# Kernel tuning notes

Hardware: AMD Instinct MI355X
Metric: run time of the kernel (lower is better)

The kernel has to match this reference:

```python
import jax, jax.numpy as jnp
import numpy as np

B, S, D = 1, 2048, 2048
HQ, HKV = 32, 8
HD = D // HQ          # 64
G = HQ // HKV         # 4 query heads per kv head


def apply_rope(x, freq):
    # x: (b, h, s, hd); freq: (s, hd//2) angles. Llama-style pairwise rotation.
    cos = jnp.cos(freq)  # (s, hd//2)
    sin = jnp.sin(freq)
    xr = x.reshape(*x.shape[:-1], HD // 2, 2)
    xe, xo = xr[..., 0], xr[..., 1]
    re = xe * cos - xo * sin
    ro = xe * sin + xo * cos
    return jnp.stack([re, ro], axis=-1).reshape(x.shape)


def setup_inputs() -> dict:
    key = jax.random.key(0)
    k1, k2, k3, k4, k5 = jax.random.split(key, 5)
    x = jax.random.normal(k1, (B, S, D), dtype=jnp.float32)
    # RoPE angles: pos * inv_freq, theta=10000
    inv_freq = 1.0 / (10000.0 ** (jnp.arange(0, HD, 2, dtype=jnp.float32) / HD))
    freq = jnp.arange(S, dtype=jnp.float32)[:, None] * inv_freq[None, :]  # (S, HD//2)
    mask = jnp.tril(jnp.ones((S, S), dtype=jnp.int32))
    scale = D ** -0.5
    wq = jax.random.normal(k2, (D, HQ * HD), dtype=jnp.float32) * scale
    wk = jax.random.normal(k3, (D, HKV * HD), dtype=jnp.float32) * scale
    wv = jax.random.normal(k4, (D, HKV * HD), dtype=jnp.float32) * scale
    wo = jax.random.normal(k5, (HQ * HD, D), dtype=jnp.float32) * scale
    return {"x": x, "freq": freq, "mask": mask, "wq": wq, "wk": wk, "wv": wv, "wo": wo}


def reference(x, freq, mask, wq, wk, wv, wo):
    b, s, d = x.shape
    q = (x @ wq).reshape(b, s, HQ, HD).transpose(0, 2, 1, 3)    # (b,HQ,s,hd)
    k = (x @ wk).reshape(b, s, HKV, HD).transpose(0, 2, 1, 3)   # (b,HKV,s,hd)
    v = (x @ wv).reshape(b, s, HKV, HD).transpose(0, 2, 1, 3)
    q = apply_rope(q, freq[:s])
    k = apply_rope(k, freq[:s])
    # GQA: broadcast kv heads over groups instead of repeat_interleave
    qg = q.reshape(b, HKV, G, s, HD)
    scores = jnp.einsum('bhgsd,bhtd->bhgst', qg, k)             # (b,HKV,G,s,s)
    scores = jnp.where(mask[:s, :s] == 0, -jnp.inf, scores)
    w = jax.nn.softmax(scores * (HD ** -0.5), axis=-1)
    out = jnp.einsum('bhgst,bhtd->bhgsd', w, v)
    out = out.reshape(b, HQ, s, HD).transpose(0, 2, 1, 3).reshape(b, s, HQ * HD)
    return out @ wo
```

## Files before the change

### kernel.cpp

```cpp
#include <hip/hip_runtime.h>

typedef unsigned short u16;
typedef unsigned int u32;
typedef unsigned long long u64;

using bf16x8 = __bf16 __attribute__((ext_vector_type(8)));
using f32x4  = float  __attribute__((ext_vector_type(4)));

#define LDS_SPACE __attribute__((address_space(3)))
#define GLB_SPACE __attribute__((address_space(1)))

static __device__ __forceinline__ u16 f2bf(float f) {
  union { float f; u32 u; } c; c.f = f;
  u32 u = c.u;
  return (u16)((u + 0x7fffu + ((u >> 16) & 1u)) >> 16);
}
static __device__ __forceinline__ float bf2f(u16 u) {
  union { u32 u; float f; } c; c.u = ((u32)u) << 16;
  return c.f;
}

static __device__ __forceinline__ void fence_barrier() {
  asm volatile("" ::: "memory");
  __builtin_amdgcn_s_barrier();
  asm volatile("" ::: "memory");
}

constexpr float SC = 0.18033688011112042f;

__device__ __constant__ unsigned char kItems[40] = {
  12, 28, 29, 42, 44, 45, 46, 57, 59, 60, 61, 62, 63,
  24, 25, 37, 38, 40, 41, 49, 51, 52, 53, 54, 55, 56, 58,
  8, 20, 21, 32, 33, 34, 36, 48, 50,
  16, 17,
  4,
  0
};

__global__ __launch_bounds__(256) void prep_k(const float* __restrict__ x,
                                              const float* __restrict__ wq,
                                              const float* __restrict__ wk,
                                              const float* __restrict__ wv,
                                              const float* __restrict__ wo,
                                              u16* __restrict__ x_bf,
                                              u16* __restrict__ wqkv_t,
                                              u16* __restrict__ wo_t) {
  const int b = blockIdx.x;
  if (b < 4096) {
    int i = b * 256 + threadIdx.x;
    float4 v = ((const float4*)x)[i];
    ushort4 o;
    o.x = f2bf(v.x); o.y = f2bf(v.y); o.z = f2bf(v.z); o.w = f2bf(v.w);
    ((ushort4*)x_bf)[i] = o;
    return;
  }
  const float* src; u16* dst; int C, bx, by; float scale = 1.0f;
  if (b < 8192)      { src = wq; dst = wqkv_t; C = 2048; int t = b - 4096; bx = t & 63; by = t >> 6; scale = SC; }
  else if (b < 9216) { src = wk; dst = wqkv_t + (size_t)2048 * 2048; C = 512; int t = b - 8192; bx = t & 15; by = t >> 4; }
  else if (b < 10240){ src = wv; dst = wqkv_t + (size_t)2560 * 2048; C = 512; int t = b - 9216; bx = t & 15; by = t >> 4; }
  else               { src = wo; dst = wo_t; C = 2048; int t = b - 10240; bx = t & 63; by = t >> 6; }
  __shared__ float t[32][33];
  const int lx = threadIdx.x & 31, ly = threadIdx.x >> 5;
  const int r0 = by * 32, c0 = bx * 32;
  #pragma unroll
  for (int i = 0; i < 32; i += 8)
    t[ly + i][lx] = src[(size_t)(r0 + ly + i) * C + c0 + lx];
  __syncthreads();
  #pragma unroll
  for (int i = 0; i < 32; i += 8)
    dst[(size_t)(c0 + ly + i) * 2048 + r0 + lx] = f2bf(t[lx][ly + i] * scale);
}

__global__ __launch_bounds__(256) void ropevt_k(u16* __restrict__ Y,
                                                const float* __restrict__ freq,
                                                u16* __restrict__ Vt) {
  const int b = blockIdx.x;
  if (b < 10240) {
    int idx = b * 256 + threadIdx.x;
    int s = idx / 1280;
    int rem = idx - s * 1280;
    int h = rem >> 5;
    int i = rem & 31;
    int col = (h < 32) ? (h * 64 + 2 * i) : (2048 + (h - 32) * 64 + 2 * i);
    float ang = freq[s * 32 + i];
    float sn, cs;
    sincosf(ang, &sn, &cs);
    size_t base = (size_t)s * 3072 + col;
    float e = bf2f(Y[base]), o = bf2f(Y[base + 1]);
    Y[base]     = f2bf(e * cs - o * sn);
    Y[base + 1] = f2bf(e * sn + o * cs);
    return;
  }
  __shared__ u16 t[64][72];
  const int tb = b - 10240;
  const int s0 = (tb & 31) * 64;
  const int c0 = (tb >> 5) * 64;
  const int lx = threadIdx.x & 63, ly = threadIdx.x >> 6;
  #pragma unroll
  for (int i = 0; i < 64; i += 4)
    t[i + ly][lx] = Y[(size_t)(s0 + i + ly) * 3072 + 2560 + c0 + lx];
  __syncthreads();
  #pragma unroll
  for (int i = 0; i < 64; i += 4)
    Vt[(size_t)(c0 + i + ly) * 2048 + s0 + lx] = t[lx][i + ly];
}

template <typename OutT, int BN, int GX>
__global__ __launch_bounds__(256) void gemm64_k(const u16* __restrict__ A,
                                                const u16* __restrict__ Bt,
                                                OutT* __restrict__ C,
                                                int M, int N, int K) {
  constexpr int WN = BN / 32;
  __shared__ u16 As[2][64 * 64];
  __shared__ u16 Bs[2][BN * 64];
  const int tid = threadIdx.x, lane = tid & 63, w = tid >> 6;
  const int wr = w >> 1, wc = w & 1;
  const int nwg = gridDim.x;
  const int bsw = (blockIdx.x & 7) * (nwg >> 3) + ((int)blockIdx.x >> 3);
  const int bm = bsw / GX, bn = bsw - bm * GX;
  const int l15 = lane & 15, lq = lane >> 4;
  f32x4 acc[2][WN] = {};

  const int srow8 = lane >> 3;
  const int scolb = ((lane & 7) ^ srow8) * 16;
  const u16* AgR = A + (size_t)(bm * 64 + w * 16 + srow8) * K;
  const u16* BgR = Bt + (size_t)(bn * BN + w * (BN / 4) + srow8) * K;

  auto stage = [&](int buf, int k0) {
    #pragma unroll
    for (int i = 0; i < 2; ++i)
      __builtin_amdgcn_global_load_lds(
          (const GLB_SPACE u32*)((const char*)(AgR + (size_t)i * 8 * K + k0) + scolb),
          (LDS_SPACE u32*)&As[buf][(w * 16 + i * 8) * 64], 16, 0, 0);
    #pragma unroll
    for (int i = 0; i < WN; ++i)
      __builtin_amdgcn_global_load_lds(
          (const GLB_SPACE u32*)((const char*)(BgR + (size_t)i * 8 * K + k0) + scolb),
          (LDS_SPACE u32*)&Bs[buf][(w * (BN / 4) + i * 8) * 64], 16, 0, 0);
  };

  stage(0, 0);
  asm volatile("s_waitcnt vmcnt(0)" ::: "memory");
  fence_barrier();

  for (int k0 = 0; k0 < K; k0 += 64) {
    const int p = (k0 >> 6) & 1;
    if (k0 + 64 < K) stage(p ^ 1, k0 + 64);

    #pragma unroll
    for (int kk = 0; kk < 2; ++kk) {
      bf16x8 a[2], b[WN];
      #pragma unroll
      for (int m = 0; m < 2; ++m) {
        const int ra = wr * 32 + m * 16 + l15;
        a[m] = *(const bf16x8*)&As[p][ra * 64 + (((kk * 4 + lq) ^ (ra & 7)) << 3)];
      }
      #pragma unroll
      for (int n = 0; n < WN; ++n) {
        const int rb = wc * (BN / 2) + n * 16 + l15;
        b[n] = *(const bf16x8*)&Bs[p][rb * 64 + (((kk * 4 + lq) ^ (rb & 7)) << 3)];
      }
      #pragma unroll
      for (int m = 0; m < 2; ++m)
        #pragma unroll
        for (int n = 0; n < WN; ++n)
          acc[m][n] = __builtin_amdgcn_mfma_f32_16x16x32_bf16(a[m], b[n], acc[m][n], 0, 0, 0);
    }

    asm volatile("s_waitcnt vmcnt(0)" ::: "memory");
    fence_barrier();
  }

  const int r0 = bm * 64 + wr * 32 + lq * 4;
  const int c0 = bn * BN + wc * (BN / 2) + l15;
  #pragma unroll
  for (int m = 0; m < 2; ++m)
    #pragma unroll
    for (int n = 0; n < WN; ++n)
      #pragma unroll
      for (int r = 0; r < 4; ++r) {
        float v = acc[m][n][r];
        size_t off = (size_t)(r0 + m * 16 + r) * N + (c0 + n * 16);
        if constexpr (sizeof(OutT) == 2) ((u16*)C)[off] = f2bf(v);
        else C[off] = v;
      }
}

__global__ __launch_bounds__(256, 3) void attn_part_k(const u16* __restrict__ Y,
                                                      const u16* __restrict__ Vtg,
                                                      u16* __restrict__ Opart,
                                                      float2* __restrict__ Ml,
                                                      u16* __restrict__ Out) {
  __shared__ u16 Ks[64 * 64];
  __shared__ u16 Vs[64 * 64];
  __shared__ u32 Ps[4][16 * 32];
  const int w = threadIdx.x >> 6, lane = threadIdx.x & 63;
  const int l15 = lane & 15, lq = lane >> 4;

  const int b = (int)blockIdx.x;
  const int head = b & 31;
  const int idx = b >> 5;
  const int v = kItems[idx];
  const int qt = v >> 2, ch = v & 3;
  const int kvh = head >> 2;
  const int ntiles = 2 * qt + 2;
  const int nch = qt < 4 ? 1 : qt < 8 ? 2 : qt < 12 ? 3 : 4;
  const int tstart = (ch * ntiles) / nch;
  const int tend = ((ch + 1) * ntiles) / nch;
  const int q0w = qt * 128 + w * 32;

  const int srow = lane >> 3;
  const int scolb = ((lane & 7) ^ srow) * 16;
  const char* gkB = (const char*)(Y + (size_t)(w * 16 + srow) * 3072 + 2048 + kvh * 64) + scolb;
  const char* gvB = (const char*)(Vtg + (size_t)(kvh * 64 + w * 16 + srow) * 2048) + scolb;

  auto stage = [&](int t) {
    const size_t t0 = (size_t)t * 64;
    #pragma unroll
    for (int i = 0; i < 2; ++i) {
      __builtin_amdgcn_global_load_lds((const GLB_SPACE u32*)(gkB + t0 * 6144 + (size_t)i * 49152),
                                       (LDS_SPACE u32*)&Ks[(w * 16 + i * 8) * 64], 16, 0, 0);
      __builtin_amdgcn_global_load_lds((const GLB_SPACE u32*)(gvB + t0 * 2 + (size_t)i * 32768),
                                       (LDS_SPACE u32*)&Vs[(w * 16 + i * 8) * 64], 16, 0, 0);
    }
  };

  int rowB[4], xk[2], pwr[4], prd[2];
  #pragma unroll
  for (int kt = 0; kt < 4; ++kt) rowB[kt] = (kt * 16 + l15) * 128;
  #pragma unroll
  for (int kk = 0; kk < 2; ++kk) xk[kk] = (((kk * 4 + lq) ^ (l15 & 7)) << 4);
  #pragma unroll
  for (int n = 0; n < 4; ++n)
    pwr[n] = (l15 * 32 + ((lq * 2 + n * 8) ^ ((l15 & 7) << 2))) * 4;
  #pragma unroll
  for (int c = 0; c < 2; ++c)
    prd[c] = l15 * 128 + (((c * 32 + lq * 8) ^ ((l15 & 7) << 3)) << 1);

  bf16x8 qf[2][2];
  #pragma unroll
  for (int qs = 0; qs < 2; ++qs)
    #pragma unroll
    for (int kk = 0; kk < 2; ++kk)
      qf[qs][kk] = *(const bf16x8*)&Y[(size_t)(q0w + qs * 16 + l15) * 3072 +
                                      head * 64 + kk * 32 + lq * 8];

  float m_[2] = { -1e30f, -1e30f };
  float l_[2] = { 0.f, 0.f };
  f32x4 accO[2][4] = {};

  for (int t = tstart; t < tend; ++t) {
    stage(t);
    asm volatile("s_waitcnt vmcnt(0)" ::: "memory");
    fence_barrier();

    const int t0 = t * 64;
    if (t0 <= q0w + 31) {
      const char* KbC = (const char*)Ks;
      const char* VbC = (const char*)Vs;

      f32x4 sc[2][4] = {};
      #pragma unroll
      for (int kk = 0; kk < 2; ++kk)
        #pragma unroll
        for (int kt = 0; kt < 4; ++kt) {
          bf16x8 a = *(const bf16x8*)(KbC + rowB[kt] + xk[kk]);
          sc[0][kt] = __builtin_amdgcn_mfma_f32_16x16x32_bf16(a, qf[0][kk], sc[0][kt], 0, 0, 0);
          sc[1][kt] = __builtin_amdgcn_mfma_f32_16x16x32_bf16(a, qf[1][kk], sc[1][kt], 0, 0, 0);
        }

      bf16x8 vf[2][4];
      #pragma unroll
      for (int c = 0; c < 2; ++c)
        #pragma unroll
        for (int dt = 0; dt < 4; ++dt)
          vf[c][dt] = *(const bf16x8*)(VbC + rowB[dt] + xk[c]);

      #pragma unroll
      for (int qs = 0; qs < 2; ++qs) {
        const int qsmin = q0w + qs * 16;
        if (t0 > qsmin + 15) continue;
        const int qrow = qsmin + l15;
        if (t0 + 63 > qsmin) {
          #pragma unroll
          for (int n = 0; n < 4; ++n)
            #pragma unroll
            for (int rr = 0; rr < 4; ++rr)
              if (t0 + n * 16 + lq * 4 + rr > qrow) sc[qs][n][rr] = -1e30f;
        }
        float a0 = fmaxf(fmaxf(sc[qs][0][0], sc[qs][0][1]), fmaxf(sc[qs][0][2], sc[qs][0][3]));
        float a1 = fmaxf(fmaxf(sc[qs][1][0], sc[qs][1][1]), fmaxf(sc[qs][1][2], sc[qs][1][3]));
        float a2 = fmaxf(fmaxf(sc[qs][2][0], sc[qs][2][1]), fmaxf(sc[qs][2][2], sc[qs][2][3]));
        float a3 = fmaxf(fmaxf(sc[qs][3][0], sc[qs][3][1]), fmaxf(sc[qs][3][2], sc[qs][3][3]));
        float mx = fmaxf(fmaxf(a0, a1), fmaxf(a2, a3));

        if (__any(mx > m_[qs] + 7.25f)) {
          float mf = mx;
          mf = fmaxf(mf, __shfl_xor(mf, 16));
          mf = fmaxf(mf, __shfl_xor(mf, 32));
          const float mnew = fmaxf(m_[qs], mf);
          const float alpha = exp2f(m_[qs] - mnew);
          l_[qs] *= alpha;
          #pragma unroll
          for (int dt = 0; dt < 4; ++dt) accO[qs][dt] *= alpha;
          m_[qs] = mnew;
        }
        const float mS = m_[qs];
        float s0 = 0.f, s1 = 0.f, s2 = 0.f, s3 = 0.f;
        char* psB = (char*)Ps[w];
        #pragma unroll
        for (int n = 0; n < 4; ++n) {
          float p0 = exp2f(sc[qs][n][0] - mS);
          float p1 = exp2f(sc[qs][n][1] - mS);
          float p2 = exp2f(sc[qs][n][2] - mS);
          float p3 = exp2f(sc[qs][n][3] - mS);
          s0 += p0; s1 += p1; s2 += p2; s3 += p3;
          u32 w0, w1;
          asm("v_cvt_pk_bf16_f32 %0, %1, %2" : "=v"(w0) : "v"(p0), "v"(p1));
          asm("v_cvt_pk_bf16_f32 %0, %1, %2" : "=v"(w1) : "v"(p2), "v"(p3));
          *(u64*)(psB + pwr[n]) = (u64)w0 | ((u64)w1 << 32);
        }
        l_[qs] += (s0 + s1) + (s2 + s3);

        #pragma unroll
        for (int c = 0; c < 2; ++c) {
          bf16x8 bb = *(const bf16x8*)(psB + prd[c]);
          #pragma unroll
          for (int dt = 0; dt < 4; ++dt)
            accO[qs][dt] = __builtin_amdgcn_mfma_f32_16x16x32_bf16(vf[c][dt], bb, accO[qs][dt], 0, 0, 0);
        }
      }
    }

    fence_barrier();
  }

  if (nch == 1) {
    #pragma unroll
    for (int qs = 0; qs < 2; ++qs) {
      float lt = l_[qs];
      lt += __shfl_xor(lt, 16);
      lt += __shfl_xor(lt, 32);
      const float rl = 1.0f / lt;
      const int qrow = q0w + qs * 16 + l15;
      #pragma unroll
      for (int dt = 0; dt < 4; ++dt) {
        ushort4 o;
        o.x = f2bf(accO[qs][dt][0] * rl);
        o.y = f2bf(accO[qs][dt][1] * rl);
        o.z = f2bf(accO[qs][dt][2] * rl);
        o.w = f2bf(accO[qs][dt][3] * rl);
        *(ushort4*)&Out[(size_t)qrow * 2048 + head * 64 + dt * 16 + lq * 4] = o;
      }
    }
    return;
  }

  const int off = qt < 8 ? (qt - 4) * 2 : qt < 12 ? 8 + (qt - 8) * 3 : 20 + (qt - 12) * 4;
  const int slot = head * 36 + off + ch;
  u16* ob = Opart + (size_t)slot * 8192;
  #pragma unroll
  for (int qs = 0; qs < 2; ++qs) {
    float lt = l_[qs];
    lt += __shfl_xor(lt, 16);
    lt += __shfl_xor(lt, 32);
    const int row = w * 32 + qs * 16 + l15;
    #pragma unroll
    for (int dt = 0; dt < 4; ++dt) {
      ushort4 o;
      o.x = f2bf(accO[qs][dt][0]);
      o.y = f2bf(accO[qs][dt][1]);
      o.z = f2bf(accO[qs][dt][2]);
      o.w = f2bf(accO[qs][dt][3]);
      *(ushort4*)&ob[row * 64 + dt * 16 + lq * 4] = o;
    }
    if (lq == 0) Ml[(size_t)slot * 128 + row] = make_float2(m_[qs], lt);
  }
}

__global__ __launch_bounds__(256) void attn_comb_k(const u16* __restrict__ Opart,
                                                   const float2* __restrict__ Ml,
                                                   u16* __restrict__ Out) {
  const int b = blockIdx.x;
  const int rg = b & 3;
  const int hq = b >> 2;
  const int head = hq / 12;
  const int qt = (hq - head * 12) + 4;
  const int nch = qt < 8 ? 2 : qt < 12 ? 3 : 4;
  const int off = qt < 8 ? (qt - 4) * 2 : qt < 12 ? 8 + (qt - 8) * 3 : 20 + (qt - 12) * 4;
  const int slot0 = head * 36 + off;
  const int rl = threadIdx.x >> 3;
  const int d8 = (threadIdx.x & 7) * 8;
  const int row = rg * 32 + rl;

  float gm = -1e30f;
  #pragma unroll 4
  for (int c = 0; c < nch; ++c)
    gm = fmaxf(gm, Ml[(size_t)(slot0 + c) * 128 + row].x);
  float den = 0.f;
  float num[8] = {};
  #pragma unroll 4
  for (int c = 0; c < nch; ++c) {
    float2 ml = Ml[(size_t)(slot0 + c) * 128 + row];
    float a = exp2f(ml.x - gm);
    den += a * ml.y;
    const u16* p = &Opart[(size_t)(slot0 + c) * 8192 + row * 64 + d8];
    ushort4 p0 = *(const ushort4*)p;
    ushort4 p1 = *(const ushort4*)(p + 4);
    num[0] += a * bf2f(p0.x); num[1] += a * bf2f(p0.y);
    num[2] += a * bf2f(p0.z); num[3] += a * bf2f(p0.w);
    num[4] += a * bf2f(p1.x); num[5] += a * bf2f(p1.y);
    num[6] += a * bf2f(p1.z); num[7] += a * bf2f(p1.w);
  }
  const float rd = 1.0f / den;
  ushort4 o0, o1;
  o0.x = f2bf(num[0] * rd); o0.y = f2bf(num[1] * rd);
  o0.z = f2bf(num[2] * rd); o0.w = f2bf(num[3] * rd);
  o1.x = f2bf(num[4] * rd); o1.y = f2bf(num[5] * rd);
  o1.z = f2bf(num[6] * rd); o1.w = f2bf(num[7] * rd);
  u16* op = &Out[(size_t)(qt * 128 + row) * 2048 + head * 64 + d8];
  *(ushort4*)op = o0;
  *(ushort4*)(op + 4) = o1;
}

extern "C" void kernel_launch(void* const* d_in, const int* in_sizes, int n_in,
                              void* d_out, int out_size, void* d_ws, size_t ws_size,
                              hipStream_t stream) {
  const float* x    = (const float*)d_in[0];
  const float* freq = (const float*)d_in[1];
  const float* wq   = (const float*)d_in[3];
  const float* wk   = (const float*)d_in[4];
  const float* wv   = (const float*)d_in[5];
  const float* wo   = (const float*)d_in[6];
  float* out = (float*)d_out;

  u16* x_bf   = (u16*)d_ws;
  u16* wqkv_t = x_bf + (size_t)2048 * 2048;
  u16* wo_t   = wqkv_t + (size_t)3072 * 2048;
  u16* y      = wo_t + (size_t)2048 * 2048;
  u16* attn   = y + (size_t)2048 * 3072;
  u16* vt     = x_bf;
  u16* opart  = attn + (size_t)2048 * 2048;
  float2* ml  = (float2*)(opart + (size_t)1152 * 8192);

  prep_k<<<14336, 256, 0, stream>>>(x, wq, wk, wv, wo, x_bf, wqkv_t, wo_t);
  gemm64_k<u16, 128, 24><<<768, 256, 0, stream>>>(x_bf, wqkv_t, y, 2048, 3072, 2048);
  ropevt_k<<<10496, 256, 0, stream>>>(y, freq, vt);
  attn_part_k<<<1280, 256, 0, stream>>>(y, vt, opart, ml, attn);
  attn_comb_k<<<1536, 256, 0, stream>>>(opart, ml, attn);
  gemm64_k<float, 64, 32><<<1024, 256, 0, stream>>>(attn, wo_t, out, 2048, 2048, 2048);
}
```

Measured before the change: 134.5 us.

## Split attention into single-wave blocks with per-32-row KV chunking

Restructures the attention partial kernel from 256-thread blocks over 128 query rows into 64-thread single-wave blocks over 32 query rows. Each block now handles up to 8 KV tiles, chosen by a closed-form work mapping instead of a lookup table. Block-wide barriers become a single-wave LDS wait, and the combine kernel is reindexed to the finer 32-row slots. The aim is better load balance and no cross-wave synchronisation. The cost is that each wave stages its full K/V tiles alone, losing K/V reuse across the four waves of a block, with more partial slots to combine.

```diff
diff --git a/kernel.cpp b/kernel.cpp
--- a/kernel.cpp
+++ b/kernel.cpp
@@ -27,15 +27,6 @@
 }
 
 constexpr float SC = 0.18033688011112042f;
-
-__device__ __constant__ unsigned char kItems[40] = {
-  12, 28, 29, 42, 44, 45, 46, 57, 59, 60, 61, 62, 63,
-  24, 25, 37, 38, 40, 41, 49, 51, 52, 53, 54, 55, 56, 58,
-  8, 20, 21, 32, 33, 34, 36, 48, 50,
-  16, 17,
-  4,
-  0
-};
 
 __global__ __launch_bounds__(256) void prep_k(const float* __restrict__ x,
                                               const float* __restrict__ wq,
@@ -186,42 +177,46 @@
       }
 }
 
-__global__ __launch_bounds__(256, 3) void attn_part_k(const u16* __restrict__ Y,
-                                                      const u16* __restrict__ Vtg,
-                                                      u16* __restrict__ Opart,
-                                                      float2* __restrict__ Ml,
-                                                      u16* __restrict__ Out) {
+__global__ __launch_bounds__(64) void attn_part_k(const u16* __restrict__ Y,
+                                                  const u16* __restrict__ Vtg,
+                                                  u16* __restrict__ Opart,
+                                                  float2* __restrict__ Ml,
+                                                  u16* __restrict__ Out) {
   __shared__ u16 Ks[64 * 64];
   __shared__ u16 Vs[64 * 64];
-  __shared__ u32 Ps[4][16 * 32];
-  const int w = threadIdx.x >> 6, lane = threadIdx.x & 63;
+  __shared__ u32 Ps[16 * 32];
+  const int lane = threadIdx.x;
   const int l15 = lane & 15, lq = lane >> 4;
 
-  const int b = (int)blockIdx.x;
-  const int head = b & 31;
-  const int idx = b >> 5;
-  const int v = kItems[idx];
-  const int qt = v >> 2, ch = v & 3;
+  const int item = 5119 - (int)blockIdx.x;
+  const int head = item / 160;
+  const int u = item - head * 160;
+  int g, r;
+  if (u < 16)      { g = 0; r = u; }
+  else if (u < 48) { g = 1; r = u - 16; }
+  else if (u < 96) { g = 2; r = u - 48; }
+  else             { g = 3; r = u - 96; }
+  const int ws = g * 16 + r / (g + 1);
+  const int ch = r - (r / (g + 1)) * (g + 1);
   const int kvh = head >> 2;
-  const int ntiles = 2 * qt + 2;
-  const int nch = qt < 4 ? 1 : qt < 8 ? 2 : qt < 12 ? 3 : 4;
-  const int tstart = (ch * ntiles) / nch;
-  const int tend = ((ch + 1) * ntiles) / nch;
-  const int q0w = qt * 128 + w * 32;
+  const int q0w = ws * 32;
+  const int ntiles = (ws + 2) >> 1;
+  const int tstart = ch * 8;
+  const int tend = min(tstart + 8, ntiles);
 
   const int srow = lane >> 3;
   const int scolb = ((lane & 7) ^ srow) * 16;
-  const char* gkB = (const char*)(Y + (size_t)(w * 16 + srow) * 3072 + 2048 + kvh * 64) + scolb;
-  const char* gvB = (const char*)(Vtg + (size_t)(kvh * 64 + w * 16 + srow) * 2048) + scolb;
+  const char* gkB = (const char*)(Y + (size_t)srow * 3072 + 2048 + kvh * 64) + scolb;
+  const char* gvB = (const char*)(Vtg + (size_t)(kvh * 64 + srow) * 2048) + scolb;
 
   auto stage = [&](int t) {
     const size_t t0 = (size_t)t * 64;
     #pragma unroll
-    for (int i = 0; i < 2; ++i) {
+    for (int i = 0; i < 8; ++i) {
       __builtin_amdgcn_global_load_lds((const GLB_SPACE u32*)(gkB + t0 * 6144 + (size_t)i * 49152),
-                                       (LDS_SPACE u32*)&Ks[(w * 16 + i * 8) * 64], 16, 0, 0);
+                                       (LDS_SPACE u32*)&Ks[i * 8 * 64], 16, 0, 0);
       __builtin_amdgcn_global_load_lds((const GLB_SPACE u32*)(gvB + t0 * 2 + (size_t)i * 32768),
-                                       (LDS_SPACE u32*)&Vs[(w * 16 + i * 8) * 64], 16, 0, 0);
+                                       (LDS_SPACE u32*)&Vs[i * 8 * 64], 16, 0, 0);
     }
   };
 
@@ -250,92 +245,89 @@
   f32x4 accO[2][4] = {};
 
   for (int t = tstart; t < tend; ++t) {
+    asm volatile("s_waitcnt lgkmcnt(0)" ::: "memory");
     stage(t);
     asm volatile("s_waitcnt vmcnt(0)" ::: "memory");
-    fence_barrier();
+    __builtin_amdgcn_sched_barrier(0);
 
     const int t0 = t * 64;
-    if (t0 <= q0w + 31) {
-      const char* KbC = (const char*)Ks;
-      const char* VbC = (const char*)Vs;
-
-      f32x4 sc[2][4] = {};
-      #pragma unroll
-      for (int kk = 0; kk < 2; ++kk)
+    const char* KbC = (const char*)Ks;
+    const char* VbC = (const char*)Vs;
+
+    f32x4 sc[2][4] = {};
+    #pragma unroll
+    for (int kk = 0; kk < 2; ++kk)
+      #pragma unroll
+      for (int kt = 0; kt < 4; ++kt) {
+        bf16x8 a = *(const bf16x8*)(KbC + rowB[kt] + xk[kk]);
+        sc[0][kt] = __builtin_amdgcn_mfma_f32_16x16x32_bf16(a, qf[0][kk], sc[0][kt], 0, 0, 0);
+        sc[1][kt] = __builtin_amdgcn_mfma_f32_16x16x32_bf16(a, qf[1][kk], sc[1][kt], 0, 0, 0);
+      }
+
+    bf16x8 vf[2][4];
+    #pragma unroll
+    for (int c = 0; c < 2; ++c)
+      #pragma unroll
+      for (int dt = 0; dt < 4; ++dt)
+        vf[c][dt] = *(const bf16x8*)(VbC + rowB[dt] + xk[c]);
+
+    #pragma unroll
+    for (int qs = 0; qs < 2; ++qs) {
+      const int qsmin = q0w + qs * 16;
+      if (t0 > qsmin + 15) continue;
+      const int qrow = qsmin + l15;
+      if (t0 + 63 > qsmin) {
         #pragma unroll
-        for (int kt = 0; kt < 4; ++kt) {
-          bf16x8 a = *(const bf16x8*)(KbC + rowB[kt] + xk[kk]);
-          sc[0][kt] = __builtin_amdgcn_mfma_f32_16x16x32_bf16(a, qf[0][kk], sc[0][kt], 0, 0, 0);
-          sc[1][kt] = __builtin_amdgcn_mfma_f32_16x16x32_bf16(a, qf[1][kk], sc[1][kt], 0, 0, 0);
-        }
-
-      bf16x8 vf[2][4];
-      #pragma unroll
-      for (int c = 0; c < 2; ++c)
+        for (int n = 0; n < 4; ++n)
+          #pragma unroll
+          for (int rr = 0; rr < 4; ++rr)
+            if (t0 + n * 16 + lq * 4 + rr > qrow) sc[qs][n][rr] = -1e30f;
+      }
+      float a0 = fmaxf(fmaxf(sc[qs][0][0], sc[qs][0][1]), fmaxf(sc[qs][0][2], sc[qs][0][3]));
+      float a1 = fmaxf(fmaxf(sc[qs][1][0], sc[qs][1][1]), fmaxf(sc[qs][1][2], sc[qs][1][3]));
+      float a2 = fmaxf(fmaxf(sc[qs][2][0], sc[qs][2][1]), fmaxf(sc[qs][2][2], sc[qs][2][3]));
+      float a3 = fmaxf(fmaxf(sc[qs][3][0], sc[qs][3][1]), fmaxf(sc[qs][3][2], sc[qs][3][3]));
+      float mx = fmaxf(fmaxf(a0, a1), fmaxf(a2, a3));
+
+      if (__any(mx > m_[qs] + 7.25f)) {
+        float mf = mx;
+        mf = fmaxf(mf, __shfl_xor(mf, 16));
+        mf = fmaxf(mf, __shfl_xor(mf, 32));
+        const float mnew = fmaxf(m_[qs], mf);
+        const float alpha = exp2f(m_[qs] - mnew);
+        l_[qs] *= alpha;
+        #pragma unroll
+        for (int dt = 0; dt < 4; ++dt) accO[qs][dt] *= alpha;
+        m_[qs] = mnew;
+      }
+      const float mS = m_[qs];
+      float s0 = 0.f, s1 = 0.f, s2 = 0.f, s3 = 0.f;
+      char* psB = (char*)Ps;
+      #pragma unroll
+      for (int n = 0; n < 4; ++n) {
+        float p0 = exp2f(sc[qs][n][0] - mS);
+        float p1 = exp2f(sc[qs][n][1] - mS);
+        float p2 = exp2f(sc[qs][n][2] - mS);
+        float p3 = exp2f(sc[qs][n][3] - mS);
+        s0 += p0; s1 += p1; s2 += p2; s3 += p3;
+        u32 w0, w1;
+        asm("v_cvt_pk_bf16_f32 %0, %1, %2" : "=v"(w0) : "v"(p0), "v"(p1));
+        asm("v_cvt_pk_bf16_f32 %0, %1, %2" : "=v"(w1) : "v"(p2), "v"(p3));
+        *(u64*)(psB + pwr[n]) = (u64)w0 | ((u64)w1 << 32);
+      }
+      l_[qs] += (s0 + s1) + (s2 + s3);
+
+      #pragma unroll
+      for (int c = 0; c < 2; ++c) {
+        bf16x8 bb = *(const bf16x8*)(psB + prd[c]);
         #pragma unroll
         for (int dt = 0; dt < 4; ++dt)
-          vf[c][dt] = *(const bf16x8*)(VbC + rowB[dt] + xk[c]);
-
-      #pragma unroll
-      for (int qs = 0; qs < 2; ++qs) {
-        const int qsmin = q0w + qs * 16;
-        if (t0 > qsmin + 15) continue;
-        const int qrow = qsmin + l15;
-        if (t0 + 63 > qsmin) {
-          #pragma unroll
-          for (int n = 0; n < 4; ++n)
-            #pragma unroll
-            for (int rr = 0; rr < 4; ++rr)
-              if (t0 + n * 16 + lq * 4 + rr > qrow) sc[qs][n][rr] = -1e30f;
-        }
-        float a0 = fmaxf(fmaxf(sc[qs][0][0], sc[qs][0][1]), fmaxf(sc[qs][0][2], sc[qs][0][3]));
-        float a1 = fmaxf(fmaxf(sc[qs][1][0], sc[qs][1][1]), fmaxf(sc[qs][1][2], sc[qs][1][3]));
-        float a2 = fmaxf(fmaxf(sc[qs][2][0], sc[qs][2][1]), fmaxf(sc[qs][2][2], sc[qs][2][3]));
-        float a3 = fmaxf(fmaxf(sc[qs][3][0], sc[qs][3][1]), fmaxf(sc[qs][3][2], sc[qs][3][3]));
-        float mx = fmaxf(fmaxf(a0, a1), fmaxf(a2, a3));
-
-        if (__any(mx > m_[qs] + 7.25f)) {
-          float mf = mx;
-          mf = fmaxf(mf, __shfl_xor(mf, 16));
-          mf = fmaxf(mf, __shfl_xor(mf, 32));
-          const float mnew = fmaxf(m_[qs], mf);
-          const float alpha = exp2f(m_[qs] - mnew);
-          l_[qs] *= alpha;
-          #pragma unroll
-          for (int dt = 0; dt < 4; ++dt) accO[qs][dt] *= alpha;
-          m_[qs] = mnew;
-        }
-        const float mS = m_[qs];
-        float s0 = 0.f, s1 = 0.f, s2 = 0.f, s3 = 0.f;
-        char* psB = (char*)Ps[w];
-        #pragma unroll
-        for (int n = 0; n < 4; ++n) {
-          float p0 = exp2f(sc[qs][n][0] - mS);
-          float p1 = exp2f(sc[qs][n][1] - mS);
-          float p2 = exp2f(sc[qs][n][2] - mS);
-          float p3 = exp2f(sc[qs][n][3] - mS);
-          s0 += p0; s1 += p1; s2 += p2; s3 += p3;
-          u32 w0, w1;
-          asm("v_cvt_pk_bf16_f32 %0, %1, %2" : "=v"(w0) : "v"(p0), "v"(p1));
-          asm("v_cvt_pk_bf16_f32 %0, %1, %2" : "=v"(w1) : "v"(p2), "v"(p3));
-          *(u64*)(psB + pwr[n]) = (u64)w0 | ((u64)w1 << 32);
-        }
-        l_[qs] += (s0 + s1) + (s2 + s3);
-
-        #pragma unroll
-        for (int c = 0; c < 2; ++c) {
-          bf16x8 bb = *(const bf16x8*)(psB + prd[c]);
-          #pragma unroll
-          for (int dt = 0; dt < 4; ++dt)
-            accO[qs][dt] = __builtin_amdgcn_mfma_f32_16x16x32_bf16(vf[c][dt], bb, accO[qs][dt], 0, 0, 0);
-        }
+          accO[qs][dt] = __builtin_amdgcn_mfma_f32_16x16x32_bf16(vf[c][dt], bb, accO[qs][dt], 0, 0, 0);
       }
     }
-
-    fence_barrier();
-  }
-
-  if (nch == 1) {
+  }
+
+  if (g == 0) {
     #pragma unroll
     for (int qs = 0; qs < 2; ++qs) {
       float lt = l_[qs];
@@ -356,15 +348,15 @@
     return;
   }
 
-  const int off = qt < 8 ? (qt - 4) * 2 : qt < 12 ? 8 + (qt - 8) * 3 : 20 + (qt - 12) * 4;
-  const int slot = head * 36 + off + ch;
-  u16* ob = Opart + (size_t)slot * 8192;
+  const int off = ws < 32 ? (ws - 16) * 2 : ws < 48 ? 32 + (ws - 32) * 3 : 80 + (ws - 48) * 4;
+  const int slot = head * 144 + off + ch;
+  u16* ob = Opart + (size_t)slot * 2048;
   #pragma unroll
   for (int qs = 0; qs < 2; ++qs) {
     float lt = l_[qs];
     lt += __shfl_xor(lt, 16);
     lt += __shfl_xor(lt, 32);
-    const int row = w * 32 + qs * 16 + l15;
+    const int row = qs * 16 + l15;
     #pragma unroll
     for (int dt = 0; dt < 4; ++dt) {
       ushort4 o;
@@ -374,7 +366,7 @@
       o.w = f2bf(accO[qs][dt][3]);
       *(ushort4*)&ob[row * 64 + dt * 16 + lq * 4] = o;
     }
-    if (lq == 0) Ml[(size_t)slot * 128 + row] = make_float2(m_[qs], lt);
+    if (lq == 0) Ml[(size_t)slot * 32 + row] = make_float2(m_[qs], lt);
   }
 }
 
@@ -382,29 +374,29 @@
                                                    const float2* __restrict__ Ml,
                                                    u16* __restrict__ Out) {
   const int b = blockIdx.x;
-  const int rg = b & 3;
-  const int hq = b >> 2;
-  const int head = hq / 12;
-  const int qt = (hq - head * 12) + 4;
-  const int nch = qt < 8 ? 2 : qt < 12 ? 3 : 4;
-  const int off = qt < 8 ? (qt - 4) * 2 : qt < 12 ? 8 + (qt - 8) * 3 : 20 + (qt - 12) * 4;
-  const int slot0 = head * 36 + off;
+  const int head = b / 48;
+  const int wsi = b - head * 48;
+  const int ws = wsi + 16;
+  int off, nch;
+  if (ws < 32)      { off = (ws - 16) * 2;    nch = 2; }
+  else if (ws < 48) { off = 32 + (ws - 32) * 3; nch = 3; }
+  else              { off = 80 + (ws - 48) * 4; nch = 4; }
+  const int slot0 = head * 144 + off;
   const int rl = threadIdx.x >> 3;
   const int d8 = (threadIdx.x & 7) * 8;
-  const int row = rg * 32 + rl;
 
   float gm = -1e30f;
   #pragma unroll 4
   for (int c = 0; c < nch; ++c)
-    gm = fmaxf(gm, Ml[(size_t)(slot0 + c) * 128 + row].x);
+    gm = fmaxf(gm, Ml[(size_t)(slot0 + c) * 32 + rl].x);
   float den = 0.f;
   float num[8] = {};
   #pragma unroll 4
   for (int c = 0; c < nch; ++c) {
-    float2 ml = Ml[(size_t)(slot0 + c) * 128 + row];
+    float2 ml = Ml[(size_t)(slot0 + c) * 32 + rl];
     float a = exp2f(ml.x - gm);
     den += a * ml.y;
-    const u16* p = &Opart[(size_t)(slot0 + c) * 8192 + row * 64 + d8];
+    const u16* p = &Opart[(size_t)(slot0 + c) * 2048 + rl * 64 + d8];
     ushort4 p0 = *(const ushort4*)p;
     ushort4 p1 = *(const ushort4*)(p + 4);
     num[0] += a * bf2f(p0.x); num[1] += a * bf2f(p0.y);
@@ -418,7 +410,7 @@
   o0.z = f2bf(num[2] * rd); o0.w = f2bf(num[3] * rd);
   o1.x = f2bf(num[4] * rd); o1.y = f2bf(num[5] * rd);
   o1.z = f2bf(num[6] * rd); o1.w = f2bf(num[7] * rd);
-  u16* op = &Out[(size_t)(qt * 128 + row) * 2048 + head * 64 + d8];
+  u16* op = &Out[(size_t)(ws * 32 + rl) * 2048 + head * 64 + d8];
   *(ushort4*)op = o0;
   *(ushort4*)(op + 4) = o1;
 }
@@ -441,12 +433,12 @@
   u16* attn   = y + (size_t)2048 * 3072;
   u16* vt     = x_bf;
   u16* opart  = attn + (size_t)2048 * 2048;
-  float2* ml  = (float2*)(opart + (size_t)1152 * 8192);
+  float2* ml  = (float2*)(opart + (size_t)4608 * 2048);
 
   prep_k<<<14336, 256, 0, stream>>>(x, wq, wk, wv, wo, x_bf, wqkv_t, wo_t);
   gemm64_k<u16, 128, 24><<<768, 256, 0, stream>>>(x_bf, wqkv_t, y, 2048, 3072, 2048);
   ropevt_k<<<10496, 256, 0, stream>>>(y, freq, vt);
-  attn_part_k<<<1280, 256, 0, stream>>>(y, vt, opart, ml, attn);
+  attn_part_k<<<5120, 64, 0, stream>>>(y, vt, opart, ml, attn);
   attn_comb_k<<<1536, 256, 0, stream>>>(opart, ml, attn);
   gemm64_k<float, 64, 32><<<1024, 256, 0, stream>>>(attn, wo_t, out, 2048, 2048, 2048);
 }
```

Result: slower. 152.9 us (+13.7%).
